# Optimization experiments

Hardware: AMD Instinct MI355X
Metric: run time of the kernel (lower is better)

Reference implementation:

```python
import jax, jax.numpy as jnp
import numpy as np

H, FFN, E, TOPK = 1024, 4096, 8, 2
B, S = 2, 1024


def setup_inputs() -> dict:
    key = jax.random.key(0)
    k1, k2, k3, k4 = jax.random.split(key, 4)
    s_h = 1.0 / np.sqrt(H).astype(np.float32)
    s_f = 1.0 / np.sqrt(FFN).astype(np.float32)
    return {
        "hidden_states": jax.random.normal(k1, (B, S, H), jnp.float32),
        "gate_w": jax.random.normal(k2, (E, H), jnp.float32) * s_h,       # router Linear(H->E), no bias
        "w13": jax.random.normal(k3, (E, 2 * FFN, H), jnp.float32) * s_h,  # fused [w1; w3] per expert
        "w2": jax.random.normal(k4, (E, H, FFN), jnp.float32) * s_f,       # down-proj per expert
        "top_k": TOPK,
    }


def reference(hidden_states, gate_w, w13, w2, top_k):
    b, s, h = hidden_states.shape
    x = hidden_states.reshape(-1, h)                       # [T, H]
    router_logits = x @ gate_w.T                           # [T, E]
    rw = jax.nn.softmax(router_logits.astype(jnp.float32), axis=1)
    rw, sel = jax.lax.top_k(rw, top_k)                     # [T, K] each
    rw = rw / rw.sum(axis=-1, keepdims=True)
    rw = rw.astype(x.dtype)
    e_tot = gate_w.shape[0]
    f = w2.shape[2]
    # combine[t, e] = sum_k rw[t, k] * (sel[t, k] == e)
    combine = jnp.sum((sel[..., None] == jnp.arange(e_tot)) * rw[..., None], axis=1)  # [T, E]
    out = jnp.zeros_like(x)
    for e in range(e_tot):  # static small loop over experts
        g = x @ w13[e, :f].T            # [T, F] gate proj
        u = x @ w13[e, f:].T            # [T, F] up proj
        y = (jax.nn.silu(g) * u) @ w2[e].T  # [T, H]
        out = out + combine[:, e:e + 1] * y
    return out.reshape(b, s, h), router_logits
```

## Files before the change

kernel.cpp:

```cpp
#include <hip/hip_runtime.h>
#include <hip/hip_bf16.h>
#include <math.h>

#define H     1024
#define FFN   4096
#define NE    8
#define TOK   2048
#define PAIRS (TOK*2)
#define BM    128
#define BK    32
#define ROWCAP (PAIRS + NE*BM)
#define MAXTILES (ROWCAP/BM)

typedef unsigned short u16;
typedef __attribute__((ext_vector_type(8))) __bf16 bf16x8;
typedef __attribute__((ext_vector_type(4))) float  f32x4;

__device__ __forceinline__ unsigned cvt2(float a, float b) {
    __hip_bfloat162 h = __float22bfloat162_rn(float2{a, b});
    unsigned u;
    __builtin_memcpy(&u, &h, 4);
    return u;
}

#define GLD16(gp, lp) __builtin_amdgcn_global_load_lds( \
    (const __attribute__((address_space(1))) void*)(gp), \
    (__attribute__((address_space(3))) void*)(lp), 16, 0, 0)

__global__ void k_init(int* counts) {
    if (threadIdx.x < NE) counts[threadIdx.x] = 0;
}

__global__ void k_router(const float* __restrict__ x, const float* __restrict__ gw,
                         float* __restrict__ logits, int* counts,
                         int* __restrict__ sel, int* __restrict__ posn, float* __restrict__ wgt) {
    int lane = threadIdx.x & 63;
    int t = blockIdx.x * 4 + (threadIdx.x >> 6);
    float p[NE];
#pragma unroll
    for (int e = 0; e < NE; e++) p[e] = 0.f;
    for (int j = 0; j < H / 64; j++) {
        int h = lane + j * 64;
        float xv = x[(size_t)t * H + h];
#pragma unroll
        for (int e = 0; e < NE; e++) p[e] = fmaf(xv, gw[e * H + h], p[e]);
    }
#pragma unroll
    for (int off = 32; off; off >>= 1)
#pragma unroll
        for (int e = 0; e < NE; e++) p[e] += __shfl_xor(p[e], off, 64);
    if (lane == 0) {
        float mx = p[0];
#pragma unroll
        for (int e = 1; e < NE; e++) mx = fmaxf(mx, p[e]);
        float pe[NE];
#pragma unroll
        for (int e = 0; e < NE; e++) pe[e] = __expf(p[e] - mx);
        int i0 = 0;
#pragma unroll
        for (int e = 1; e < NE; e++) if (pe[e] > pe[i0]) i0 = e;
        int i1 = (i0 == 0) ? 1 : 0;
#pragma unroll
        for (int e = 0; e < NE; e++) if (e != i1 && e != i0 && pe[e] > pe[i1]) i1 = e;
        float w0 = pe[i0] / (pe[i0] + pe[i1]);
#pragma unroll
        for (int e = 0; e < NE; e++) logits[(size_t)t * NE + e] = p[e];
        int p0 = atomicAdd(&counts[i0], 1);
        int p1 = atomicAdd(&counts[i1], 1);
        sel[2 * t] = i0;  posn[2 * t] = p0;  wgt[2 * t] = w0;
        sel[2 * t + 1] = i1;  posn[2 * t + 1] = p1;  wgt[2 * t + 1] = 1.f - w0;
    }
}

__global__ void k_prefix(const int* __restrict__ counts, int* __restrict__ base,
                         int* __restrict__ tile_e) {
    if (threadIdx.x == 0) {
        int b = 0, tb = 0;
        for (int e = 0; e < NE; e++) {
            base[e] = b;
            int nt = (counts[e] + BM - 1) / BM;
            for (int i = 0; i < nt; i++) tile_e[tb++] = e;
            b += nt * BM;
        }
        base[NE] = b;
        while (tb < MAXTILES) tile_e[tb++] = -1;
    }
}

__global__ void k_gather(const float4* __restrict__ x4, const int* __restrict__ sel,
                         const int* __restrict__ posn, const int* __restrict__ base,
                         u16* __restrict__ xg) {
    int p = blockIdx.x;
    int lane = threadIdx.x;
    int t = p >> 1;
    int row = base[sel[p]] + posn[p];
#pragma unroll
    for (int i = 0; i < 4; i++) {
        int idx = i * 64 + lane;
        float4 v = x4[(size_t)t * (H / 4) + idx];
        uint2 o = { cvt2(v.x, v.y), cvt2(v.z, v.w) };
        *(uint2*)&xg[(size_t)row * H + idx * 4] = o;
    }
}

__global__ __launch_bounds__(256) void k_gemm1(const u16* __restrict__ xg,
                                               const float* __restrict__ w13,
                                               u16* __restrict__ act,
                                               const int* __restrict__ tile_e) {
    int e = tile_e[blockIdx.x];
    if (e < 0) return;
    __shared__ u16 As[BM * BK];
    __shared__ u16 Bs[2][64 * (BK + 8)];

    int tid = threadIdx.x;
    int lane = tid & 63, wave = tid >> 6;
    int quad = lane >> 4, m16 = lane & 15;
    int wm = wave >> 1, wn = wave & 1;
    int row0 = blockIdx.x * BM;
    int n0 = blockIdx.y * 64;
    const float* wb1 = w13 + ((size_t)e * 2 * FFN + n0) * H;
    const float* wb3 = w13 + ((size_t)e * 2 * FFN + FFN + n0) * H;

    f32x4 accg[4][2], accu[4][2];
#pragma unroll
    for (int mi = 0; mi < 4; mi++)
#pragma unroll
        for (int ni = 0; ni < 2; ni++) { accg[mi][ni] = {0.f,0.f,0.f,0.f}; accu[mi][ni] = {0.f,0.f,0.f,0.f}; }

    for (int kk = 0; kk < H; kk += BK) {
#pragma unroll
        for (int i = 0; i < 2; i++) {
            int chunk = i * 256 + tid;
            int r = chunk >> 2, c = (chunk & 3) * 8;
            GLD16(xg + (size_t)(row0 + r) * H + kk + c, As + chunk * 8);
        }
#pragma unroll
        for (int i = 0; i < 2; i++) {
            int idx = i * 256 + tid;
            int r = idx >> 3, c4 = idx & 7;
            float4 v1 = *(const float4*)(wb1 + (size_t)r * H + kk + c4 * 4);
            float4 v3 = *(const float4*)(wb3 + (size_t)r * H + kk + c4 * 4);
            uint2 o1 = { cvt2(v1.x, v1.y), cvt2(v1.z, v1.w) };
            uint2 o3 = { cvt2(v3.x, v3.y), cvt2(v3.z, v3.w) };
            *(uint2*)&Bs[0][r * (BK + 8) + c4 * 4] = o1;
            *(uint2*)&Bs[1][r * (BK + 8) + c4 * 4] = o3;
        }
        __syncthreads();
        bf16x8 a[4], bg[2], bu[2];
#pragma unroll
        for (int mi = 0; mi < 4; mi++)
            a[mi] = *(const bf16x8*)&As[(wm * 64 + mi * 16 + m16) * BK + quad * 8];
#pragma unroll
        for (int ni = 0; ni < 2; ni++) {
            bg[ni] = *(const bf16x8*)&Bs[0][(wn * 32 + ni * 16 + m16) * (BK + 8) + quad * 8];
            bu[ni] = *(const bf16x8*)&Bs[1][(wn * 32 + ni * 16 + m16) * (BK + 8) + quad * 8];
        }
#pragma unroll
        for (int mi = 0; mi < 4; mi++)
#pragma unroll
            for (int ni = 0; ni < 2; ni++) {
                accg[mi][ni] = __builtin_amdgcn_mfma_f32_16x16x32_bf16(a[mi], bg[ni], accg[mi][ni], 0, 0, 0);
                accu[mi][ni] = __builtin_amdgcn_mfma_f32_16x16x32_bf16(a[mi], bu[ni], accu[mi][ni], 0, 0, 0);
            }
        __syncthreads();
    }
#pragma unroll
    for (int mi = 0; mi < 4; mi++)
#pragma unroll
        for (int ni = 0; ni < 2; ni++) {
            int gcol = n0 + wn * 32 + ni * 16 + m16;
            int grow = row0 + wm * 64 + mi * 16 + quad * 4;
#pragma unroll
            for (int r = 0; r < 4; r++) {
                float g = accg[mi][ni][r], u = accu[mi][ni][r];
                float hv = g * (1.f / (1.f + __expf(-g))) * u;
                unsigned pk = cvt2(hv, hv);
                act[(size_t)(grow + r) * FFN + gcol] = (u16)(pk & 0xffff);
            }
        }
}

__global__ __launch_bounds__(256) void k_gemm2(const u16* __restrict__ act,
                                               const float* __restrict__ w2,
                                               float* __restrict__ yc,
                                               const int* __restrict__ tile_e) {
    int e = tile_e[blockIdx.x];
    if (e < 0) return;
    __shared__ u16 As[BM * BK];
    __shared__ u16 Bs[BM * (BK + 8)];

    int tid = threadIdx.x;
    int lane = tid & 63, wave = tid >> 6;
    int quad = lane >> 4, m16 = lane & 15;
    int wm = wave >> 1, wn = wave & 1;
    int row0 = blockIdx.x * BM;
    int n0 = blockIdx.y * 128;
    int k0 = blockIdx.z * (FFN / 2);
    const float* wb = w2 + ((size_t)e * H + n0) * FFN;
    float* ycp = yc + (size_t)blockIdx.z * ROWCAP * H;

    f32x4 acc[4][4];
#pragma unroll
    for (int mi = 0; mi < 4; mi++)
#pragma unroll
        for (int ni = 0; ni < 4; ni++) acc[mi][ni] = {0.f,0.f,0.f,0.f};

    for (int kk = k0; kk < k0 + FFN / 2; kk += BK) {
#pragma unroll
        for (int i = 0; i < 2; i++) {
            int chunk = i * 256 + tid;
            int r = chunk >> 2, c = (chunk & 3) * 8;
            GLD16(act + (size_t)(row0 + r) * FFN + kk + c, As + chunk * 8);
        }
#pragma unroll
        for (int i = 0; i < 4; i++) {
            int idx = i * 256 + tid;
            int r = idx >> 3, c4 = idx & 7;
            float4 v = *(const float4*)(wb + (size_t)r * FFN + kk + c4 * 4);
            uint2 o = { cvt2(v.x, v.y), cvt2(v.z, v.w) };
            *(uint2*)&Bs[r * (BK + 8) + c4 * 4] = o;
        }
        __syncthreads();
        bf16x8 a[4], b[4];
#pragma unroll
        for (int mi = 0; mi < 4; mi++)
            a[mi] = *(const bf16x8*)&As[(wm * 64 + mi * 16 + m16) * BK + quad * 8];
#pragma unroll
        for (int ni = 0; ni < 4; ni++)
            b[ni] = *(const bf16x8*)&Bs[(wn * 64 + ni * 16 + m16) * (BK + 8) + quad * 8];
#pragma unroll
        for (int mi = 0; mi < 4; mi++)
#pragma unroll
            for (int ni = 0; ni < 4; ni++)
                acc[mi][ni] = __builtin_amdgcn_mfma_f32_16x16x32_bf16(a[mi], b[ni], acc[mi][ni], 0, 0, 0);
        __syncthreads();
    }
#pragma unroll
    for (int mi = 0; mi < 4; mi++)
#pragma unroll
        for (int ni = 0; ni < 4; ni++)
#pragma unroll
            for (int r = 0; r < 4; r++) {
                int grow = row0 + wm * 64 + mi * 16 + quad * 4 + r;
                int gcol = n0 + wn * 64 + ni * 16 + m16;
                ycp[(size_t)grow * H + gcol] = acc[mi][ni][r];
            }
}

__global__ void k_combine(const float4* __restrict__ yc4, const int* __restrict__ sel,
                          const int* __restrict__ posn, const int* __restrict__ base,
                          const float* __restrict__ wgt, float4* __restrict__ out4) {
    int t = blockIdx.x;
    int j = threadIdx.x;
    int r0 = base[sel[2 * t]] + posn[2 * t];
    int r1 = base[sel[2 * t + 1]] + posn[2 * t + 1];
    float w0 = wgt[2 * t], w1 = wgt[2 * t + 1];
    const size_t P = (size_t)ROWCAP * (H / 4);
    float4 a0 = yc4[(size_t)r0 * (H / 4) + j];
    float4 a1 = yc4[(size_t)r0 * (H / 4) + j + P];
    float4 b0 = yc4[(size_t)r1 * (H / 4) + j];
    float4 b1 = yc4[(size_t)r1 * (H / 4) + j + P];
    float4 o = { w0 * (a0.x + a1.x) + w1 * (b0.x + b1.x),
                 w0 * (a0.y + a1.y) + w1 * (b0.y + b1.y),
                 w0 * (a0.z + a1.z) + w1 * (b0.z + b1.z),
                 w0 * (a0.w + a1.w) + w1 * (b0.w + b1.w) };
    out4[(size_t)t * (H / 4) + j] = o;
}

extern "C" void kernel_launch(void* const* d_in, const int* in_sizes, int n_in,
                              void* d_out, int out_size, void* d_ws, size_t ws_size,
                              hipStream_t stream) {
    const float* x   = (const float*)d_in[0];
    const float* gw  = (const float*)d_in[1];
    const float* w13 = (const float*)d_in[2];
    const float* w2  = (const float*)d_in[3];
    float* out    = (float*)d_out;
    float* logits = out + (size_t)TOK * H;

    char* ws = (char*)d_ws;
    int*   counts = (int*)ws;
    int*   base   = (int*)(ws + 256);
    int*   tile_e = (int*)(ws + 512);
    int*   sel    = (int*)(ws + 1024);
    int*   posn   = (int*)(ws + 1024 + 4 * PAIRS);
    float* wgt    = (float*)(ws + 1024 + 8 * PAIRS);
    u16*   xg     = (u16*)(ws + 65536);
    u16*   act    = xg + (size_t)ROWCAP * H;
    float* yc     = (float*)(act + (size_t)ROWCAP * FFN);

    k_init<<<1, 64, 0, stream>>>(counts);
    k_router<<<TOK / 4, 256, 0, stream>>>(x, gw, logits, counts, sel, posn, wgt);
    k_prefix<<<1, 64, 0, stream>>>(counts, base, tile_e);
    k_gather<<<PAIRS, 64, 0, stream>>>((const float4*)x, sel, posn, base, xg);
    dim3 g1(MAXTILES, FFN / 64);
    k_gemm1<<<g1, 256, 0, stream>>>(xg, w13, act, tile_e);
    dim3 g2(MAXTILES, H / 128, 2);
    k_gemm2<<<g2, 256, 0, stream>>>(act, w2, yc, tile_e);
    k_combine<<<TOK, 256, 0, stream>>>((const float4*)yc, sel, posn, base, wgt, (float4*)out);
}
```

Baseline: 720.0 us.

## Pre-convert expert weights to bf16 and stream them into LDS directly

Adds a conversion kernel that turns all w13 and w2 fp32 weights into bf16 copies in the workspace once per call. Both GEMMs then load A and B tiles with direct global-to-LDS 16-byte loads instead of fp32 register loads followed by in-loop conversion, and the LDS row padding is dropped. This removes repeated fp32 weight traffic and conversion work across M-tiles. The cost is a full extra pass over the weights on every call and a larger workspace, with the yc buffer reusing the w13b region. Dropping the padding may also introduce LDS bank conflicts.

```diff
diff --git a/kernel.cpp b/kernel.cpp
--- a/kernel.cpp
+++ b/kernel.cpp
@@ -26,6 +26,20 @@
 #define GLD16(gp, lp) __builtin_amdgcn_global_load_lds( \
     (const __attribute__((address_space(1))) void*)(gp), \
     (__attribute__((address_space(3))) void*)(lp), 16, 0, 0)
+
+__global__ __launch_bounds__(256) void k_cvtw(const float4* __restrict__ w13,
+                                              const float4* __restrict__ w2,
+                                              uint4* __restrict__ o13,
+                                              uint4* __restrict__ o2) {
+    size_t i = (size_t)blockIdx.x * 256 + threadIdx.x;
+    const size_t N13 = (size_t)NE * 2 * FFN * H / 8;
+    const float4* src; uint4* dst; size_t j;
+    if (i < N13) { src = w13; dst = o13; j = i; }
+    else         { src = w2;  dst = o2;  j = i - N13; }
+    float4 a = src[2 * j], b = src[2 * j + 1];
+    uint4 o = { cvt2(a.x, a.y), cvt2(a.z, a.w), cvt2(b.x, b.y), cvt2(b.z, b.w) };
+    dst[j] = o;
+}
 
 __global__ void k_init(int* counts) {
     if (threadIdx.x < NE) counts[threadIdx.x] = 0;
@@ -104,13 +118,13 @@
 }
 
 __global__ __launch_bounds__(256) void k_gemm1(const u16* __restrict__ xg,
-                                               const float* __restrict__ w13,
+                                               const u16* __restrict__ w13b,
                                                u16* __restrict__ act,
                                                const int* __restrict__ tile_e) {
     int e = tile_e[blockIdx.x];
     if (e < 0) return;
     __shared__ u16 As[BM * BK];
-    __shared__ u16 Bs[2][64 * (BK + 8)];
+    __shared__ u16 Bs[BM * BK];
 
     int tid = threadIdx.x;
     int lane = tid & 63, wave = tid >> 6;
@@ -118,8 +132,8 @@
     int wm = wave >> 1, wn = wave & 1;
     int row0 = blockIdx.x * BM;
     int n0 = blockIdx.y * 64;
-    const float* wb1 = w13 + ((size_t)e * 2 * FFN + n0) * H;
-    const float* wb3 = w13 + ((size_t)e * 2 * FFN + FFN + n0) * H;
+    const u16* wb1 = w13b + ((size_t)e * 2 * FFN + n0) * H;
+    const u16* wb3 = w13b + ((size_t)e * 2 * FFN + FFN + n0) * H;
 
     f32x4 accg[4][2], accu[4][2];
 #pragma unroll
@@ -127,24 +141,12 @@
 #pragma unroll
         for (int ni = 0; ni < 2; ni++) { accg[mi][ni] = {0.f,0.f,0.f,0.f}; accu[mi][ni] = {0.f,0.f,0.f,0.f}; }
 
+    int r4 = tid >> 2, c8 = (tid & 3) * 8;
     for (int kk = 0; kk < H; kk += BK) {
-#pragma unroll
-        for (int i = 0; i < 2; i++) {
-            int chunk = i * 256 + tid;
-            int r = chunk >> 2, c = (chunk & 3) * 8;
-            GLD16(xg + (size_t)(row0 + r) * H + kk + c, As + chunk * 8);
-        }
-#pragma unroll
-        for (int i = 0; i < 2; i++) {
-            int idx = i * 256 + tid;
-            int r = idx >> 3, c4 = idx & 7;
-            float4 v1 = *(const float4*)(wb1 + (size_t)r * H + kk + c4 * 4);
-            float4 v3 = *(const float4*)(wb3 + (size_t)r * H + kk + c4 * 4);
-            uint2 o1 = { cvt2(v1.x, v1.y), cvt2(v1.z, v1.w) };
-            uint2 o3 = { cvt2(v3.x, v3.y), cvt2(v3.z, v3.w) };
-            *(uint2*)&Bs[0][r * (BK + 8) + c4 * 4] = o1;
-            *(uint2*)&Bs[1][r * (BK + 8) + c4 * 4] = o3;
-        }
+        GLD16(xg + (size_t)(row0 + r4) * H + kk + c8, As + tid * 8);
+        GLD16(xg + (size_t)(row0 + 64 + r4) * H + kk + c8, As + 2048 + tid * 8);
+        GLD16(wb1 + (size_t)r4 * H + kk + c8, Bs + tid * 8);
+        GLD16(wb3 + (size_t)r4 * H + kk + c8, Bs + 2048 + tid * 8);
         __syncthreads();
         bf16x8 a[4], bg[2], bu[2];
 #pragma unroll
@@ -152,8 +154,8 @@
             a[mi] = *(const bf16x8*)&As[(wm * 64 + mi * 16 + m16) * BK + quad * 8];
 #pragma unroll
         for (int ni = 0; ni < 2; ni++) {
-            bg[ni] = *(const bf16x8*)&Bs[0][(wn * 32 + ni * 16 + m16) * (BK + 8) + quad * 8];
-            bu[ni] = *(const bf16x8*)&Bs[1][(wn * 32 + ni * 16 + m16) * (BK + 8) + quad * 8];
+            bg[ni] = *(const bf16x8*)&Bs[(wn * 32 + ni * 16 + m16) * BK + quad * 8];
+            bu[ni] = *(const bf16x8*)&Bs[2048 + (wn * 32 + ni * 16 + m16) * BK + quad * 8];
         }
 #pragma unroll
         for (int mi = 0; mi < 4; mi++)
@@ -181,13 +183,13 @@
 }
 
 __global__ __launch_bounds__(256) void k_gemm2(const u16* __restrict__ act,
-                                               const float* __restrict__ w2,
+                                               const u16* __restrict__ w2b,
                                                float* __restrict__ yc,
                                                const int* __restrict__ tile_e) {
     int e = tile_e[blockIdx.x];
     if (e < 0) return;
     __shared__ u16 As[BM * BK];
-    __shared__ u16 Bs[BM * (BK + 8)];
+    __shared__ u16 Bs[BM * BK];
 
     int tid = threadIdx.x;
     int lane = tid & 63, wave = tid >> 6;
@@ -196,7 +198,7 @@
     int row0 = blockIdx.x * BM;
     int n0 = blockIdx.y * 128;
     int k0 = blockIdx.z * (FFN / 2);
-    const float* wb = w2 + ((size_t)e * H + n0) * FFN;
+    const u16* wb = w2b + ((size_t)e * H + n0) * FFN;
     float* ycp = yc + (size_t)blockIdx.z * ROWCAP * H;
 
     f32x4 acc[4][4];
@@ -205,21 +207,12 @@
 #pragma unroll
         for (int ni = 0; ni < 4; ni++) acc[mi][ni] = {0.f,0.f,0.f,0.f};
 
+    int r4 = tid >> 2, c8 = (tid & 3) * 8;
     for (int kk = k0; kk < k0 + FFN / 2; kk += BK) {
-#pragma unroll
-        for (int i = 0; i < 2; i++) {
-            int chunk = i * 256 + tid;
-            int r = chunk >> 2, c = (chunk & 3) * 8;
-            GLD16(act + (size_t)(row0 + r) * FFN + kk + c, As + chunk * 8);
-        }
-#pragma unroll
-        for (int i = 0; i < 4; i++) {
-            int idx = i * 256 + tid;
-            int r = idx >> 3, c4 = idx & 7;
-            float4 v = *(const float4*)(wb + (size_t)r * FFN + kk + c4 * 4);
-            uint2 o = { cvt2(v.x, v.y), cvt2(v.z, v.w) };
-            *(uint2*)&Bs[r * (BK + 8) + c4 * 4] = o;
-        }
+        GLD16(act + (size_t)(row0 + r4) * FFN + kk + c8, As + tid * 8);
+        GLD16(act + (size_t)(row0 + 64 + r4) * FFN + kk + c8, As + 2048 + tid * 8);
+        GLD16(wb + (size_t)r4 * FFN + kk + c8, Bs + tid * 8);
+        GLD16(wb + (size_t)(64 + r4) * FFN + kk + c8, Bs + 2048 + tid * 8);
         __syncthreads();
         bf16x8 a[4], b[4];
 #pragma unroll
@@ -227,7 +220,7 @@
             a[mi] = *(const bf16x8*)&As[(wm * 64 + mi * 16 + m16) * BK + quad * 8];
 #pragma unroll
         for (int ni = 0; ni < 4; ni++)
-            b[ni] = *(const bf16x8*)&Bs[(wn * 64 + ni * 16 + m16) * (BK + 8) + quad * 8];
+            b[ni] = *(const bf16x8*)&Bs[(wn * 64 + ni * 16 + m16) * BK + quad * 8];
 #pragma unroll
         for (int mi = 0; mi < 4; mi++)
 #pragma unroll
@@ -286,15 +279,19 @@
     float* wgt    = (float*)(ws + 1024 + 8 * PAIRS);
     u16*   xg     = (u16*)(ws + 65536);
     u16*   act    = xg + (size_t)ROWCAP * H;
-    float* yc     = (float*)(act + (size_t)ROWCAP * FFN);
-
+    u16*   w13b   = act + (size_t)ROWCAP * FFN;
+    u16*   w2b    = w13b + (size_t)NE * 2 * FFN * H;
+    float* yc     = (float*)w13b;
+
+    k_cvtw<<<49152, 256, 0, stream>>>((const float4*)w13, (const float4*)w2,
+                                      (uint4*)w13b, (uint4*)w2b);
     k_init<<<1, 64, 0, stream>>>(counts);
     k_router<<<TOK / 4, 256, 0, stream>>>(x, gw, logits, counts, sel, posn, wgt);
     k_prefix<<<1, 64, 0, stream>>>(counts, base, tile_e);
     k_gather<<<PAIRS, 64, 0, stream>>>((const float4*)x, sel, posn, base, xg);
     dim3 g1(MAXTILES, FFN / 64);
-    k_gemm1<<<g1, 256, 0, stream>>>(xg, w13, act, tile_e);
+    k_gemm1<<<g1, 256, 0, stream>>>(xg, w13b, act, tile_e);
     dim3 g2(MAXTILES, H / 128, 2);
-    k_gemm2<<<g2, 256, 0, stream>>>(act, w2, yc, tile_e);
+    k_gemm2<<<g2, 256, 0, stream>>>(act, w2b, yc, tile_e);
     k_combine<<<TOK, 256, 0, stream>>>((const float4*)yc, sel, posn, base, wgt, (float4*)out);
 }
```

Result: slower. 758.1 us (+5.3%).
